# Kernel optimization log

Measured on AMD Instinct MI355X. Metric: run time of the kernel, lower is better.

The kernel has to match this reference:

```python
import jax, jax.numpy as jnp
import numpy as np

L, D, HID, QH, KVH, V, B, S, R = 2, 1024, 4096, 16, 4, 32000, 2, 2048, 20
HEAD, G = D // QH, QH // KVH
ALPHA, THETA = 32.0, 50000.0


def setup_inputs() -> dict:
    key = jax.random.key(0)
    ks = iter(jax.random.split(key, 40))
    def w(shape, s=0.02):
        return jax.random.normal(next(ks), shape, jnp.float32) * s
    KD = KVH * HEAD
    return {
        'xs': jax.random.randint(next(ks), (B, S), 0, V, dtype=jnp.int32),
        'emb': w((V, D)),
        'Wq': w((L, D, D)), 'bq': w((L, D)),
        'Wk': w((L, D, KD)), 'bk': w((L, KD)),
        'Wv': w((L, D, KD)), 'bv': w((L, KD)),
        'Wo': w((L, D, D)), 'bo': w((L, D)),
        'att_scale': 1.0 + w((L, D)),
        'mlp_scale': 1.0 + w((L, D)),
        'final_scale': 1.0 + w((D,)),
        'W1': w((L, D, HID)), 'A1': w((L, D, R)), 'a1b': w((L, R)), 'B1': w((L, R, HID)), 'b1b': w((L, HID)),
        'W2': w((L, D, HID)), 'A2': w((L, D, R)), 'a2b': w((L, R)), 'B2': w((L, R, HID)), 'b2b': w((L, HID)),
        'W3': w((L, HID, D)), 'A3': w((L, HID, R)), 'a3b': w((L, R)), 'B3': w((L, R, D)), 'b3b': w((L, D)),
        'startpos': 0,
    }


def _rms(x, scale):
    return scale * x * jax.lax.rsqrt(jnp.mean(x * x, axis=-1, keepdims=True) + 1e-5)


def _lora(x, Wl, Aw, ab, Bw, bb):
    # base linear output is detached in the original (no grad through it)
    return jax.lax.stop_gradient(x @ Wl) + ((x @ Aw + ab) @ Bw + bb) / ALPHA


def _forward(xs, startpos, emb, Wq, bq, Wk, bk, Wv, bv, Wo, bo,
             att_scale, mlp_scale, final_scale,
             W1, A1, a1b, B1, b1b, W2, A2, a2b, B2, b2b, W3, A3, a3b, B3, b3b):
    x = emb[xs]  # (B,S,D)
    # RoPE tables (head dim = D//QH, pairs rotated as complex numbers)
    freqs = 1.0 / THETA ** (jnp.arange(0, HEAD, 2, dtype=jnp.float32) / HEAD)  # (HEAD//2,)
    pos = jnp.arange(startpos, startpos + S, dtype=jnp.float32)
    ang = pos[:, None] * freqs[None, :]  # (S, HEAD//2)
    cos, sin = jnp.cos(ang), jnp.sin(ang)

    def rope(t):  # t: (B,S,H,HEAD)
        tr = t.reshape(t.shape[:-1] + (HEAD // 2, 2))
        t0, t1 = tr[..., 0], tr[..., 1]
        c, s = cos[None, :, None, :], sin[None, :, None, :]
        return jnp.stack((t0 * c - t1 * s, t0 * s + t1 * c), axis=-1).reshape(t.shape)

    causal = jnp.arange(S)[None, :] <= jnp.arange(S)[:, None]  # (Sq, Skv)
    inv_sqrt_d = np.float32(1.0 / np.sqrt(HEAD))
    for l in range(L):
        h = _rms(x, att_scale[l])
        q = rope((h @ Wq[l] + bq[l]).reshape(B, S, QH, HEAD))
        k = rope((h @ Wk[l] + bk[l]).reshape(B, S, KVH, HEAD))
        v = (h @ Wv[l] + bv[l]).reshape(B, S, KVH, HEAD)
        # GQA: q heads grouped per kv head (q head i uses kv head i//G); no explicit KV repeat
        qg = q.reshape(B, S, KVH, G, HEAD)
        scores = jnp.einsum('bskgd,btkd->bkgst', qg, k) * inv_sqrt_d
        if startpos == 0:
            scores = jnp.where(causal[None, None, None], scores, -jnp.inf)
        attn = jax.nn.softmax(scores, axis=-1)
        o = jnp.einsum('bkgst,btkd->bskgd', attn, v).reshape(B, S, D)
        x = x + (o @ Wo[l] + bo[l])
        h2 = _rms(x, mlp_scale[l])
        m = _lora(h2, W1[l], A1[l], a1b[l], B1[l], b1b[l]) * jax.nn.silu(
            _lora(h2, W2[l], A2[l], a2b[l], B2[l], b2b[l]))
        x = x + _lora(m, W3[l], A3[l], a3b[l], B3[l], b3b[l])
    f = _rms(x, final_scale)
    return f @ emb.T  # tied logits (B,S,V)


def reference(xs, emb, Wq, bq, Wk, bk, Wv, bv, Wo, bo, att_scale, mlp_scale, final_scale,
              W1, A1, a1b, B1, b1b, W2, A2, a2b, B2, b2b, W3, A3, a3b, B3, b3b, startpos):
    return _forward(xs, startpos, emb, Wq, bq, Wk, bk, Wv, bv, Wo, bo,
                    att_scale, mlp_scale, final_scale,
                    W1, A1, a1b, B1, b1b, W2, A2, a2b, B2, b2b, W3, A3, a3b, B3, b3b)
```

## Files before the change

kernel.cpp:

```cpp
#include <hip/hip_runtime.h>
#include <hip/hip_bf16.h>
#include <math.h>

constexpr int L_   = 2;
constexpr int D_   = 1024;
constexpr int HID_ = 4096;
constexpr int QH_  = 16;
constexpr int KVH_ = 4;
constexpr int V_   = 32000;
constexpr int B_   = 2;
constexpr int S_   = 2048;
constexpr int R_   = 20;
constexpr int HEAD_ = D_ / QH_;
constexpr int KD_   = KVH_ * HEAD_;
constexpr int QKV_  = D_ + 2 * KD_;
constexpr int M_    = B_ * S_;
constexpr float INV_ALPHA_ = 1.0f / 32.0f;
constexpr float LOG_STEP_ = 0.3381180865f;

typedef unsigned short ushort_t;
typedef __attribute__((ext_vector_type(8))) short bf16x8;
typedef __attribute__((ext_vector_type(4))) float f32x4;
typedef __attribute__((address_space(1))) const unsigned int gas_u32;
typedef __attribute__((address_space(3))) unsigned int las_u32;

__device__ __forceinline__ void gload16(const void* g, void* l) {
  __builtin_amdgcn_global_load_lds((gas_u32*)g, (las_u32*)l, 16, 0, 0);
}

__device__ __forceinline__ ushort_t f2bf(float f) {
  union { float f; unsigned int u; } c; c.f = f;
  unsigned int u = c.u + 0x7FFFu + ((c.u >> 16) & 1u);
  return (ushort_t)(u >> 16);
}
__device__ __forceinline__ float bflo(unsigned int w) {
  union { unsigned int u; float f; } c; c.u = w << 16; return c.f;
}
__device__ __forceinline__ float bfhi(unsigned int w) {
  union { unsigned int u; float f; } c; c.u = w & 0xFFFF0000u; return c.f;
}

__global__ __launch_bounds__(256) void k_embed(const int* __restrict__ xs,
                                               const float* __restrict__ emb,
                                               float* __restrict__ x) {
  int i = blockIdx.x * blockDim.x + threadIdx.x;
  int total4 = M_ * D_ / 4;
  if (i >= total4) return;
  int row = i >> 8;
  int c4  = i & 255;
  const float4* src = reinterpret_cast<const float4*>(emb + (size_t)xs[row] * D_) + c4;
  reinterpret_cast<float4*>(x)[i] = *src;
}

__global__ __launch_bounds__(256) void k_rms(const float* __restrict__ x,
                                             const float* __restrict__ scale,
                                             ushort_t* __restrict__ out) {
  int row = blockIdx.x;
  const float* xr = x + (size_t)row * D_;
  float ss = 0.f;
  for (int i = threadIdx.x; i < D_; i += 256) { float v = xr[i]; ss += v * v; }
  for (int off = 32; off > 0; off >>= 1) ss += __shfl_down(ss, off);
  __shared__ float red[5];
  if ((threadIdx.x & 63) == 0) red[threadIdx.x >> 6] = ss;
  __syncthreads();
  if (threadIdx.x == 0)
    red[4] = rsqrtf((red[0] + red[1] + red[2] + red[3]) * (1.0f / D_) + 1e-5f);
  __syncthreads();
  float inv = red[4];
  ushort_t* orow = out + (size_t)row * D_;
  for (int i = threadIdx.x; i < D_; i += 256) orow[i] = f2bf(scale[i] * xr[i] * inv);
}

__global__ __launch_bounds__(256) void k_cast(const float* __restrict__ in,
                                              ushort_t* __restrict__ out, int n8) {
  int i = blockIdx.x * blockDim.x + threadIdx.x;
  if (i >= n8) return;
  const float4* p = reinterpret_cast<const float4*>(in) + i * 2;
  float4 a = p[0], b = p[1];
  ushort_t r[8] = { f2bf(a.x), f2bf(a.y), f2bf(a.z), f2bf(a.w),
                    f2bf(b.x), f2bf(b.y), f2bf(b.z), f2bf(b.w) };
  reinterpret_cast<uint4*>(out)[i] = *reinterpret_cast<uint4*>(r);
}

__global__ __launch_bounds__(256) void k_tcast(const float* __restrict__ in,
                                               ushort_t* __restrict__ out,
                                               int K, int N) {
  __shared__ float t[32][33];
  int n0 = blockIdx.x * 32, k0 = blockIdx.y * 32;
  int c = threadIdx.x & 31, r0 = threadIdx.x >> 5;
#pragma unroll
  for (int rr = 0; rr < 4; ++rr) {
    int r = r0 + rr * 8;
    t[r][c] = in[(size_t)(k0 + r) * N + n0 + c];
  }
  __syncthreads();
#pragma unroll
  for (int rr = 0; rr < 4; ++rr) {
    int r = r0 + rr * 8;
    out[(size_t)(n0 + r) * K + k0 + c] = f2bf(t[c][r]);
  }
}

__global__ __launch_bounds__(256) void k_qkvbias(const float* __restrict__ bq,
                                                 const float* __restrict__ bk,
                                                 const float* __restrict__ bv,
                                                 float* __restrict__ b) {
  int i = blockIdx.x * 256 + threadIdx.x;
  if (i >= QKV_) return;
  b[i] = i < D_ ? bq[i] : (i < D_ + KD_ ? bk[i - D_] : bv[i - D_ - KD_]);
}

__global__ __launch_bounds__(256) void k_ropeprep_k(const float* __restrict__ qkv,
                                                    ushort_t* __restrict__ Kb) {
  int i = blockIdx.x * 256 + threadIdx.x;
  int pi = i & 31;
  int kh = (i >> 5) & 3;
  int s  = (i >> 7) & (S_ - 1);
  int b  = i >> 18;
  float freq = expf(-LOG_STEP_ * (float)pi);
  float ang = (float)s * freq;
  float sn, cs;
  sincosf(ang, &sn, &cs);
  const float* p = qkv + (size_t)(b * S_ + s) * QKV_ + D_ + kh * 64 + 2 * pi;
  float t0 = p[0], t1 = p[1];
  ushort_t* q = Kb + (size_t)((b * KVH_ + kh) * S_ + s) * 64 + 2 * pi;
  q[0] = f2bf(t0 * cs - t1 * sn);
  q[1] = f2bf(t0 * sn + t1 * cs);
}

__global__ __launch_bounds__(256) void k_prep_v(const float* __restrict__ qkv,
                                                ushort_t* __restrict__ Vt) {
  __shared__ float t[32][33];
  int s0 = blockIdx.x * 32, d0 = blockIdx.y * 32, bkh = blockIdx.z;
  int c = threadIdx.x & 31, r0 = threadIdx.x >> 5;
#pragma unroll
  for (int rr = 0; rr < 4; ++rr) {
    int r = r0 + rr * 8;
    t[r][c] = qkv[(size_t)((bkh >> 2) * S_ + s0 + r) * QKV_ + D_ + KD_ + (bkh & 3) * 64 + d0 + c];
  }
  __syncthreads();
#pragma unroll
  for (int rr = 0; rr < 4; ++rr) {
    int r = r0 + rr * 8;
    Vt[(size_t)(bkh * 64 + d0 + r) * S_ + s0 + c] = f2bf(t[c][r]);
  }
}

__global__ __launch_bounds__(256) void k_attn3(const float* __restrict__ qkv,
                                               const ushort_t* __restrict__ Kb,
                                               const ushort_t* __restrict__ Vt,
                                               ushort_t* __restrict__ obf) {
  __shared__ ushort_t Ks[64 * 64];
  __shared__ ushort_t Vs[64 * 64];
  __shared__ ushort_t Ps[4][16 * 64];

  int bid = blockIdx.x;
  int qt = 31 - (bid & 31);
  int qh = (bid >> 5) & 15;
  int b  = bid >> 9;
  int kh = qh >> 2;
  int tid = threadIdx.x;
  int w = tid >> 6, lane = tid & 63;
  int q0 = qt * 64;

  const ushort_t* Kbh = Kb + (size_t)(b * KVH_ + kh) * S_ * 64;
  const ushort_t* Vth = Vt + (size_t)(b * KVH_ + kh) * 64 * S_;

  bf16x8 qa[2];
  {
    int pos = q0 + w * 16 + (lane & 15);
    const float* qp = qkv + (size_t)(b * S_ + pos) * QKV_ + qh * 64 + (lane >> 4) * 8;
#pragma unroll
    for (int kk = 0; kk < 2; ++kk) {
      float4 f0 = *reinterpret_cast<const float4*>(qp + kk * 32);
      float4 f1 = *reinterpret_cast<const float4*>(qp + kk * 32 + 4);
      float f[8] = {f0.x, f0.y, f0.z, f0.w, f1.x, f1.y, f1.z, f1.w};
      int dbase = (lane >> 4) * 8 + kk * 32;
      ushort_t tq[8];
#pragma unroll
      for (int p = 0; p < 4; ++p) {
        int pi = (dbase >> 1) + p;
        float freq = expf(-LOG_STEP_ * (float)pi);
        float ang = (float)pos * freq;
        float sn, cs;
        sincosf(ang, &sn, &cs);
        float t0 = f[2 * p], t1 = f[2 * p + 1];
        tq[2 * p]     = f2bf((t0 * cs - t1 * sn) * 0.125f);
        tq[2 * p + 1] = f2bf((t0 * sn + t1 * cs) * 0.125f);
      }
      qa[kk] = *reinterpret_cast<const bf16x8*>(tq);
    }
  }

  f32x4 oacc[4];
#pragma unroll
  for (int j = 0; j < 4; ++j) oacc[j] = {0.f, 0.f, 0.f, 0.f};
  float m[4] = {-1e30f, -1e30f, -1e30f, -1e30f};
  float l[4] = {0.f, 0.f, 0.f, 0.f};

  const int srow = lane >> 3;
  const int soff = ((lane & 7) ^ srow) * 16;

  for (int t0 = 0; t0 <= q0; t0 += 64) {
#pragma unroll
    for (int r = 0; r < 2; ++r) {
      int c = w * 2 + r;
      const char* gk = (const char*)Kbh + (size_t)(t0 + c * 8 + srow) * 128 + soff;
      gload16(gk, (char*)Ks + c * 1024);
      const char* gv = (const char*)Vth + (size_t)(c * 8 + srow) * (S_ * 2) + (size_t)t0 * 2 + soff;
      gload16(gv, (char*)Vs + c * 1024);
    }
    __syncthreads();

    f32x4 sacc[4];
#pragma unroll
    for (int j = 0; j < 4; ++j) sacc[j] = {0.f, 0.f, 0.f, 0.f};
#pragma unroll
    for (int kk = 0; kk < 2; ++kk) {
#pragma unroll
      for (int j = 0; j < 4; ++j) {
        int krow = j * 16 + (lane & 15);
        int chunk = kk * 4 + (lane >> 4);
        bf16x8 kf = *reinterpret_cast<const bf16x8*>(
            &Ks[krow * 64 + ((chunk ^ (krow & 7)) << 3)]);
        sacc[j] = __builtin_amdgcn_mfma_f32_16x16x32_bf16(qa[kk], kf, sacc[j], 0, 0, 0);
      }
    }
    if (t0 == q0) {
#pragma unroll
      for (int j = 0; j < 4; ++j)
#pragma unroll
        for (int e = 0; e < 4; ++e) {
          int keyr = j * 16 + (lane & 15);
          int qr = w * 16 + (lane >> 4) * 4 + e;
          if (keyr > qr) sacc[j][e] = -1e30f;
        }
    }

    float corr[4];
#pragma unroll
    for (int e = 0; e < 4; ++e) {
      float mt = fmaxf(fmaxf(sacc[0][e], sacc[1][e]), fmaxf(sacc[2][e], sacc[3][e]));
#pragma unroll
      for (int off = 1; off < 16; off <<= 1) mt = fmaxf(mt, __shfl_xor(mt, off));
      float mn = fmaxf(m[e], mt);
      corr[e] = __expf(m[e] - mn);
      m[e] = mn;
    }
    float rs[4] = {0.f, 0.f, 0.f, 0.f};
#pragma unroll
    for (int j = 0; j < 4; ++j)
#pragma unroll
      for (int e = 0; e < 4; ++e) {
        float p = __expf(sacc[j][e] - m[e]);
        sacc[j][e] = p;
        rs[e] += p;
      }
#pragma unroll
    for (int e = 0; e < 4; ++e) {
#pragma unroll
      for (int off = 1; off < 16; off <<= 1) rs[e] += __shfl_xor(rs[e], off);
      l[e] = l[e] * corr[e] + rs[e];
    }
#pragma unroll
    for (int j = 0; j < 4; ++j)
#pragma unroll
      for (int e = 0; e < 4; ++e) oacc[j][e] *= corr[e];

#pragma unroll
    for (int j = 0; j < 4; ++j)
#pragma unroll
      for (int e = 0; e < 4; ++e) {
        int prow = (lane >> 4) * 4 + e;
        int pcol = j * 16 + (lane & 15);
        Ps[w][prow * 64 + (((pcol >> 3) ^ (prow & 7)) << 3) + (pcol & 7)] = f2bf(sacc[j][e]);
      }

    bf16x8 pa[2];
    int prow2 = lane & 15;
#pragma unroll
    for (int kk = 0; kk < 2; ++kk) {
      int chunk = kk * 4 + (lane >> 4);
      pa[kk] = *reinterpret_cast<const bf16x8*>(
          &Ps[w][prow2 * 64 + ((chunk ^ (prow2 & 7)) << 3)]);
    }
#pragma unroll
    for (int kk = 0; kk < 2; ++kk) {
#pragma unroll
      for (int jd = 0; jd < 4; ++jd) {
        int vrow = jd * 16 + (lane & 15);
        int chunk = kk * 4 + (lane >> 4);
        bf16x8 vf = *reinterpret_cast<const bf16x8*>(
            &Vs[vrow * 64 + ((chunk ^ (vrow & 7)) << 3)]);
        oacc[jd] = __builtin_amdgcn_mfma_f32_16x16x32_bf16(pa[kk], vf, oacc[jd], 0, 0, 0);
      }
    }
    __syncthreads();
  }

#pragma unroll
  for (int e = 0; e < 4; ++e) {
    int tok = b * S_ + q0 + w * 16 + (lane >> 4) * 4 + e;
    float inv = 1.f / l[e];
#pragma unroll
    for (int jd = 0; jd < 4; ++jd) {
      int col = qh * 64 + jd * 16 + (lane & 15);
      obf[(size_t)tok * D_ + col] = f2bf(oacc[jd][e] * inv);
    }
  }
}

__global__ __launch_bounds__(256) void k_silumul(const ushort_t* __restrict__ g1,
                                                 const ushort_t* __restrict__ g2,
                                                 ushort_t* __restrict__ out) {
  int i = blockIdx.x * 256 + threadIdx.x;
  uint4 a4 = reinterpret_cast<const uint4*>(g1)[i];
  uint4 b4 = reinterpret_cast<const uint4*>(g2)[i];
  unsigned au[4] = {a4.x, a4.y, a4.z, a4.w};
  unsigned bu[4] = {b4.x, b4.y, b4.z, b4.w};
  ushort_t r[8];
#pragma unroll
  for (int q = 0; q < 4; ++q) {
    float a0 = bflo(au[q]), a1 = bfhi(au[q]);
    float b0 = bflo(bu[q]), b1 = bfhi(bu[q]);
    r[2 * q]     = f2bf(a0 * b0 / (1.f + __expf(-b0)));
    r[2 * q + 1] = f2bf(a1 * b1 / (1.f + __expf(-b1)));
  }
  reinterpret_cast<uint4*>(out)[i] = *reinterpret_cast<uint4*>(r);
}

__global__ __launch_bounds__(256) void k_trA(const float* __restrict__ A,
                                             ushort_t* __restrict__ At, int K) {
  int idx = blockIdx.x * 256 + threadIdx.x;
  if (idx >= K * R_) return;
  int k = idx / R_, r = idx - k * R_;
  At[(size_t)r * K + k] = f2bf(A[idx]);
}

template <int K>
__global__ __launch_bounds__(256) void k_loraA(const ushort_t* __restrict__ hbm,
                                               const ushort_t* __restrict__ At,
                                               const float* __restrict__ ab,
                                               float* __restrict__ u) {
  constexpr int E = K / 64;
  int row = blockIdx.x * 4 + (threadIdx.x >> 6);
  int lane = threadIdx.x & 63;
  float hf[E];
  {
    const uint4* hp = reinterpret_cast<const uint4*>(hbm + (size_t)row * K + lane * E);
#pragma unroll
    for (int i = 0; i < E / 8; ++i) {
      uint4 vv = hp[i];
      unsigned int wsv[4] = {vv.x, vv.y, vv.z, vv.w};
#pragma unroll
      for (int q = 0; q < 4; ++q) {
        hf[i * 8 + q * 2]     = bflo(wsv[q]);
        hf[i * 8 + q * 2 + 1] = bfhi(wsv[q]);
      }
    }
  }
  for (int r = 0; r < R_; ++r) {
    const uint4* ap = reinterpret_cast<const uint4*>(At + (size_t)r * K + lane * E);
    float acc = 0.f;
#pragma unroll
    for (int i = 0; i < E / 8; ++i) {
      uint4 av = ap[i];
      unsigned int wsv[4] = {av.x, av.y, av.z, av.w};
#pragma unroll
      for (int q = 0; q < 4; ++q) {
        acc = fmaf(hf[i * 8 + q * 2], bflo(wsv[q]), acc);
        acc = fmaf(hf[i * 8 + q * 2 + 1], bfhi(wsv[q]), acc);
      }
    }
#pragma unroll
    for (int off = 1; off < 64; off <<= 1) acc += __shfl_xor(acc, off);
    if (lane == 0) u[(size_t)row * R_ + r] = acc + ab[r];
  }
}

template <bool LORA, bool OBF, bool NTS>
__global__ __launch_bounds__(256) void k_bgemm(const ushort_t* __restrict__ A,
                                               const ushort_t* __restrict__ Bt,
                                               const float* __restrict__ bias,
                                               const float* __restrict__ u,
                                               const float* __restrict__ Bl,
                                               const float* __restrict__ lb,
                                               const float* __restrict__ Cin,
                                               void* __restrict__ Cout,
                                               int M, int N, int K) {
  __shared__ ushort_t lds[3][2][128 * 32];
  const int tid = threadIdx.x;
  const int lane = tid & 63;
  const int w = tid >> 6;
  const int wr = w >> 1, wc = w & 1;

  unsigned nwg = gridDim.x * gridDim.y;
  unsigned orig = blockIdx.y * gridDim.x + blockIdx.x;
  unsigned qq = nwg >> 3, r8 = nwg & 7;
  unsigned xcd = orig & 7, loc = orig >> 3;
  unsigned swz = (xcd < r8 ? xcd * (qq + 1) : r8 * (qq + 1) + (xcd - r8) * qq) + loc;
  const int bm = (int)(swz / gridDim.x) * 128;
  const int bn = (int)(swz % gridDim.x) * 128;

  f32x4 acc[4][4];
#pragma unroll
  for (int i = 0; i < 4; ++i)
#pragma unroll
    for (int j = 0; j < 4; ++j) acc[i][j] = {0.f, 0.f, 0.f, 0.f};

  const int srow = (lane >> 2);
  const int skcol = (lane & 3) * 8;
  const int nt = K >> 5;

#define STAGE_TILE(kt)                                                          \
  {                                                                             \
    int k0_ = (kt) * 32;                                                        \
    int sl_ = (kt) % 3;                                                         \
    _Pragma("unroll")                                                           \
    for (int q_ = 0; q_ < 2; ++q_) {                                            \
      int c_ = w * 2 + q_;                                                      \
      gload16(A + (size_t)(bm + c_ * 16 + srow) * K + k0_ + skcol,              \
              (char*)&lds[sl_][0][0] + c_ * 1024);                              \
      gload16(Bt + (size_t)(bn + c_ * 16 + srow) * K + k0_ + skcol,             \
              (char*)&lds[sl_][1][0] + c_ * 1024);                              \
    }                                                                           \
  }

  STAGE_TILE(0)
  STAGE_TILE(1)
  asm volatile("s_waitcnt vmcnt(4)\n\ts_barrier" ::: "memory");

  const int koff = (lane >> 4) * 8;
  const int rsel = lane & 15;

  for (int t = 0; t < nt; ++t) {
    if (t + 2 < nt) STAGE_TILE(t + 2)
    const ushort_t* As = &lds[t % 3][0][0];
    const ushort_t* Bs = &lds[t % 3][1][0];
    bf16x8 af[4], bfr[4];
#pragma unroll
    for (int i = 0; i < 4; ++i)
      af[i] = *reinterpret_cast<const bf16x8*>(&As[(wr * 64 + i * 16 + rsel) * 32 + koff]);
#pragma unroll
    for (int j = 0; j < 4; ++j)
      bfr[j] = *reinterpret_cast<const bf16x8*>(&Bs[(wc * 64 + j * 16 + rsel) * 32 + koff]);
    __builtin_amdgcn_s_setprio(1);
#pragma unroll
    for (int i = 0; i < 4; ++i)
#pragma unroll
      for (int j = 0; j < 4; ++j)
        acc[i][j] = __builtin_amdgcn_mfma_f32_16x16x32_bf16(af[i], bfr[j], acc[i][j], 0, 0, 0);
    __builtin_amdgcn_s_setprio(0);
    if (t + 2 < nt) {
      asm volatile("s_waitcnt vmcnt(4)\n\ts_barrier" ::: "memory");
    } else if (t + 1 < nt) {
      asm volatile("s_waitcnt vmcnt(0)\n\ts_barrier" ::: "memory");
    }
  }
#undef STAGE_TILE

  float* Cf = (float*)Cout;
  ushort_t* Cb = (ushort_t*)Cout;

  if constexpr (LORA) {
    asm volatile("s_barrier" ::: "memory");
    float* Us  = (float*)&lds[0][0][0];
    float* Bls = (float*)&lds[1][0][0];
    for (int t = tid; t < 128 * R_; t += 256) {
      Us[t] = u[(size_t)bm * R_ + t];
      int rr = t >> 7, nn = t & 127;
      Bls[t] = Bl[(size_t)rr * N + bn + nn];
    }
    __syncthreads();
#pragma unroll
    for (int i = 0; i < 4; ++i) {
      int rl0 = wr * 64 + i * 16 + (lane >> 4) * 4;
#pragma unroll
      for (int e = 0; e < 4; ++e) {
        int rl = rl0 + e;
        float u20[R_];
#pragma unroll
        for (int r = 0; r < R_; ++r) u20[r] = Us[rl * R_ + r];
#pragma unroll
        for (int j = 0; j < 4; ++j) {
          int cl = wc * 64 + j * 16 + (lane & 15);
          float ud = lb[bn + cl];
#pragma unroll
          for (int r = 0; r < R_; ++r) ud = fmaf(u20[r], Bls[r * 128 + cl], ud);
          int row = bm + rl, col = bn + cl;
          float vv = acc[i][j][e] + ud * INV_ALPHA_;
          if constexpr (OBF) {
            Cb[(size_t)row * N + col] = f2bf(vv);
          } else {
            if (Cin) vv += Cin[(size_t)row * N + col];
            Cf[(size_t)row * N + col] = vv;
          }
        }
      }
    }
  } else {
#pragma unroll
    for (int i = 0; i < 4; ++i) {
      int row0 = bm + wr * 64 + i * 16 + (lane >> 4) * 4;
#pragma unroll
      for (int j = 0; j < 4; ++j) {
        int col = bn + wc * 64 + j * 16 + (lane & 15);
        float bv = bias ? bias[col] : 0.f;
#pragma unroll
        for (int e = 0; e < 4; ++e) {
          int row = row0 + e;
          float vv = acc[i][j][e] + bv;
          if constexpr (OBF) {
            Cb[(size_t)row * N + col] = f2bf(vv);
          } else {
            if (Cin) vv += Cin[(size_t)row * N + col];
            if constexpr (NTS) {
              __builtin_nontemporal_store(vv, &Cf[(size_t)row * N + col]);
            } else {
              Cf[(size_t)row * N + col] = vv;
            }
          }
        }
      }
    }
  }
}

static inline void bgemm(hipStream_t st, const ushort_t* A, const ushort_t* Bt,
                         const float* bias, const float* Cin, float* C,
                         int M, int N, int K, bool nts = false) {
  dim3 g(N / 128, M / 128);
  if (nts)
    k_bgemm<false, false, true><<<g, 256, 0, st>>>(A, Bt, bias, nullptr, nullptr, nullptr, Cin, C, M, N, K);
  else
    k_bgemm<false, false, false><<<g, 256, 0, st>>>(A, Bt, bias, nullptr, nullptr, nullptr, Cin, C, M, N, K);
}
static inline void bgemm_lora_bf(hipStream_t st, const ushort_t* A, const ushort_t* Bt,
                                 const float* u, const float* Bl, const float* lb,
                                 ushort_t* C, int M, int N, int K) {
  dim3 g(N / 128, M / 128);
  k_bgemm<true, true, false><<<g, 256, 0, st>>>(A, Bt, nullptr, u, Bl, lb, nullptr, C, M, N, K);
}
static inline void bgemm_lora_f32(hipStream_t st, const ushort_t* A, const ushort_t* Bt,
                                  const float* u, const float* Bl, const float* lb,
                                  const float* Cin, float* C, int M, int N, int K) {
  dim3 g(N / 128, M / 128);
  k_bgemm<true, false, false><<<g, 256, 0, st>>>(A, Bt, nullptr, u, Bl, lb, Cin, C, M, N, K);
}
static inline void tcast(hipStream_t st, const float* in, ushort_t* out, int K, int N) {
  dim3 g(N / 32, K / 32);
  k_tcast<<<g, 256, 0, st>>>(in, out, K, N);
}

extern "C" void kernel_launch(void* const* d_in, const int* in_sizes, int n_in,
                              void* d_out, int out_size, void* d_ws, size_t ws_size,
                              hipStream_t stream) {
  (void)in_sizes; (void)n_in; (void)out_size; (void)ws_size;
  const int*   xs  = (const int*)d_in[0];
  const float* emb = (const float*)d_in[1];
  const float* Wq  = (const float*)d_in[2];
  const float* bq  = (const float*)d_in[3];
  const float* Wk  = (const float*)d_in[4];
  const float* bk  = (const float*)d_in[5];
  const float* Wv  = (const float*)d_in[6];
  const float* bv  = (const float*)d_in[7];
  const float* Wo  = (const float*)d_in[8];
  const float* bo  = (const float*)d_in[9];
  const float* att_scale   = (const float*)d_in[10];
  const float* mlp_scale   = (const float*)d_in[11];
  const float* final_scale = (const float*)d_in[12];
  const float* W1  = (const float*)d_in[13];
  const float* A1  = (const float*)d_in[14];
  const float* a1b = (const float*)d_in[15];
  const float* B1  = (const float*)d_in[16];
  const float* b1b = (const float*)d_in[17];
  const float* W2  = (const float*)d_in[18];
  const float* A2  = (const float*)d_in[19];
  const float* a2b = (const float*)d_in[20];
  const float* B2  = (const float*)d_in[21];
  const float* b2b = (const float*)d_in[22];
  const float* W3  = (const float*)d_in[23];
  const float* A3  = (const float*)d_in[24];
  const float* a3b = (const float*)d_in[25];
  const float* B3  = (const float*)d_in[26];
  const float* b3b = (const float*)d_in[27];
  float* out = (float*)d_out;

  float* ws   = (float*)d_ws;
  float* xbuf = ws;
  float* qkv  = xbuf + (size_t)M_ * D_;
  float* ubuf = qkv + (size_t)M_ * QKV_;
  float* qkvb = ubuf + (size_t)M_ * R_;
  ushort_t* g1b = (ushort_t*)(qkvb + QKV_);
  ushort_t* g2b = g1b + (size_t)M_ * HID_;
  ushort_t* hb  = g2b + (size_t)M_ * HID_;
  ushort_t* wT  = hb + (size_t)M_ * HID_;
  ushort_t* At  = wT + (size_t)HID_ * D_;
  ushort_t* embT = At + (size_t)R_ * HID_;
  ushort_t* Kb = g1b;
  ushort_t* Vt = Kb + (size_t)B_ * KVH_ * S_ * 64;

  k_embed<<<dim3(M_ * D_ / 4 / 256), dim3(256), 0, stream>>>(xs, emb, xbuf);

  for (int l = 0; l < L_; ++l) {
    k_rms<<<dim3(M_), dim3(256), 0, stream>>>(xbuf, att_scale + (size_t)l * D_, hb);
    tcast(stream, Wq + (size_t)l * D_ * D_, wT, D_, D_);
    tcast(stream, Wk + (size_t)l * D_ * KD_, wT + (size_t)D_ * D_, D_, KD_);
    tcast(stream, Wv + (size_t)l * D_ * KD_, wT + (size_t)(D_ + KD_) * D_, D_, KD_);
    k_qkvbias<<<dim3(6), dim3(256), 0, stream>>>(bq + (size_t)l * D_, bk + (size_t)l * KD_,
                                                 bv + (size_t)l * KD_, qkvb);
    bgemm(stream, hb, wT, qkvb, nullptr, qkv, M_, QKV_, D_);
    {
      int npk = M_ * KVH_ * 32;
      k_ropeprep_k<<<dim3(npk / 256), dim3(256), 0, stream>>>(qkv, Kb);
    }
    k_prep_v<<<dim3(S_ / 32, 2, B_ * KVH_), dim3(256), 0, stream>>>(qkv, Vt);
    k_attn3<<<dim3(B_ * QH_ * (S_ / 64)), dim3(256), 0, stream>>>(qkv, Kb, Vt, hb);
    tcast(stream, Wo + (size_t)l * D_ * D_, wT, D_, D_);
    bgemm(stream, hb, wT, bo + (size_t)l * D_, xbuf, xbuf, M_, D_, D_);

    k_rms<<<dim3(M_), dim3(256), 0, stream>>>(xbuf, mlp_scale + (size_t)l * D_, hb);
    k_trA<<<dim3((D_ * R_ + 255) / 256), dim3(256), 0, stream>>>(A1 + (size_t)l * D_ * R_, At, D_);
    k_loraA<D_><<<dim3(M_ / 4), dim3(256), 0, stream>>>(hb, At, a1b + (size_t)l * R_, ubuf);
    tcast(stream, W1 + (size_t)l * D_ * HID_, wT, D_, HID_);
    bgemm_lora_bf(stream, hb, wT, ubuf, B1 + (size_t)l * R_ * HID_, b1b + (size_t)l * HID_,
                  g1b, M_, HID_, D_);
    k_trA<<<dim3((D_ * R_ + 255) / 256), dim3(256), 0, stream>>>(A2 + (size_t)l * D_ * R_, At, D_);
    k_loraA<D_><<<dim3(M_ / 4), dim3(256), 0, stream>>>(hb, At, a2b + (size_t)l * R_, ubuf);
    tcast(stream, W2 + (size_t)l * D_ * HID_, wT, D_, HID_);
    bgemm_lora_bf(stream, hb, wT, ubuf, B2 + (size_t)l * R_ * HID_, b2b + (size_t)l * HID_,
                  g2b, M_, HID_, D_);
    k_silumul<<<dim3(M_ * HID_ / 8 / 256), dim3(256), 0, stream>>>(g1b, g2b, hb);
    k_trA<<<dim3((HID_ * R_ + 255) / 256), dim3(256), 0, stream>>>(A3 + (size_t)l * HID_ * R_, At, HID_);
    k_loraA<HID_><<<dim3(M_ / 4), dim3(256), 0, stream>>>(hb, At, a3b + (size_t)l * R_, ubuf);
    tcast(stream, W3 + (size_t)l * HID_ * D_, wT, HID_, D_);
    bgemm_lora_f32(stream, hb, wT, ubuf, B3 + (size_t)l * R_ * D_, b3b + (size_t)l * D_,
                   xbuf, xbuf, M_, D_, HID_);
  }

  k_rms<<<dim3(M_), dim3(256), 0, stream>>>(xbuf, final_scale, hb);
  {
    int n8 = (int)((size_t)V_ * D_ / 8);
    k_cast<<<dim3((n8 + 255) / 256), dim3(256), 0, stream>>>(emb, embT, n8);
  }
  bgemm(stream, hb, embT, nullptr, nullptr, out, M_, V_, D_, true);
}
```

Measured before the change: 1.802 ms.

## Add 256x128-tile, 512-thread GEMM with 64-wide K stages for MLP and logits

Adds a new GEMM kernel, k_bgemm2, that uses 256x128 output tiles, 8 waves, 64-deep K slices, XOR-swizzled LDS and triple-buffered async loads. It is used for the W1/W2 LoRA projections and the large vocabulary logits GEMM. The goal is more operand reuse per tile and fewer barriers per K step. It also drops the nontemporal store path for the logits output. Larger tiles raise LDS and register pressure and leave fewer workgroups for occupancy.

Result: faster. 1.566 ms (-13.1%).

```diff
diff --git a/kernel.cpp b/kernel.cpp
--- a/kernel.cpp
+++ b/kernel.cpp
@@ -378,7 +378,7 @@
   }
 }
 
-template <bool LORA, bool OBF, bool NTS>
+template <bool LORA, bool OBF>
 __global__ __launch_bounds__(256) void k_bgemm(const ushort_t* __restrict__ A,
                                                const ushort_t* __restrict__ Bt,
                                                const float* __restrict__ bias,
@@ -514,11 +514,7 @@
             Cb[(size_t)row * N + col] = f2bf(vv);
           } else {
             if (Cin) vv += Cin[(size_t)row * N + col];
-            if constexpr (NTS) {
-              __builtin_nontemporal_store(vv, &Cf[(size_t)row * N + col]);
-            } else {
-              Cf[(size_t)row * N + col] = vv;
-            }
+            Cf[(size_t)row * N + col] = vv;
           }
         }
       }
@@ -526,26 +522,186 @@
   }
 }
 
+template <bool LORA, bool OBF>
+__global__ __launch_bounds__(512, 2) void k_bgemm2(const ushort_t* __restrict__ A,
+                                                   const ushort_t* __restrict__ Bt,
+                                                   const float* __restrict__ bias,
+                                                   const float* __restrict__ u,
+                                                   const float* __restrict__ Bl,
+                                                   const float* __restrict__ lb,
+                                                   const float* __restrict__ Cin,
+                                                   void* __restrict__ Cout,
+                                                   int M, int N, int K) {
+  __shared__ ushort_t lds[3][24576];
+  const int tid = threadIdx.x;
+  const int lane = tid & 63;
+  const int w = tid >> 6;
+  const int wr = w >> 1;
+  const int wc = w & 1;
+
+  unsigned nwg = gridDim.x * gridDim.y;
+  unsigned orig = blockIdx.y * gridDim.x + blockIdx.x;
+  unsigned qq = nwg >> 3, r8 = nwg & 7;
+  unsigned xcd = orig & 7, loc = orig >> 3;
+  unsigned swz = (xcd < r8 ? xcd * (qq + 1) : r8 * (qq + 1) + (xcd - r8) * qq) + loc;
+  const int bm = (int)(swz / gridDim.x) * 256;
+  const int bn = (int)(swz % gridDim.x) * 128;
+
+  f32x4 acc[4][4];
+#pragma unroll
+  for (int i = 0; i < 4; ++i)
+#pragma unroll
+    for (int j = 0; j < 4; ++j) acc[i][j] = {0.f, 0.f, 0.f, 0.f};
+
+  const int srow8 = lane >> 3;
+  const int scol  = ((lane & 7) ^ srow8) * 8;
+  const int nt = K >> 6;
+
+#define STAGE2(kt)                                                              \
+  {                                                                             \
+    int k0_ = (kt) << 6;                                                        \
+    int sl_ = (kt) % 3;                                                         \
+    _Pragma("unroll")                                                           \
+    for (int c_ = 0; c_ < 4; ++c_) {                                            \
+      int ch = w * 4 + c_;                                                      \
+      gload16(A + (size_t)(bm + ch * 8 + srow8) * K + k0_ + scol,               \
+              (char*)&lds[sl_][0] + ch * 1024);                                 \
+    }                                                                           \
+    _Pragma("unroll")                                                           \
+    for (int c_ = 0; c_ < 2; ++c_) {                                            \
+      int ch = w * 2 + c_;                                                      \
+      gload16(Bt + (size_t)(bn + ch * 8 + srow8) * K + k0_ + scol,              \
+              (char*)&lds[sl_][16384] + ch * 1024);                             \
+    }                                                                           \
+  }
+
+  STAGE2(0)
+  STAGE2(1)
+  asm volatile("s_waitcnt vmcnt(6)\n\ts_barrier" ::: "memory");
+
+  const int rsel = lane & 15;
+  const int g4 = lane >> 4;
+
+  for (int t = 0; t < nt; ++t) {
+    if (t + 2 < nt) STAGE2(t + 2)
+    const ushort_t* As = &lds[t % 3][0];
+    const ushort_t* Bs = &lds[t % 3][16384];
+#pragma unroll
+    for (int kk = 0; kk < 2; ++kk) {
+      int slotA = kk * 4 + g4;
+      bf16x8 af[4], bfr[4];
+#pragma unroll
+      for (int fm = 0; fm < 4; ++fm) {
+        int row = wr * 64 + fm * 16 + rsel;
+        af[fm] = *reinterpret_cast<const bf16x8*>(&As[row * 64 + ((slotA ^ (row & 7)) << 3)]);
+      }
+#pragma unroll
+      for (int fn = 0; fn < 4; ++fn) {
+        int row = wc * 64 + fn * 16 + rsel;
+        bfr[fn] = *reinterpret_cast<const bf16x8*>(&Bs[row * 64 + ((slotA ^ (row & 7)) << 3)]);
+      }
+      __builtin_amdgcn_s_setprio(1);
+#pragma unroll
+      for (int fm = 0; fm < 4; ++fm)
+#pragma unroll
+        for (int fn = 0; fn < 4; ++fn)
+          acc[fm][fn] = __builtin_amdgcn_mfma_f32_16x16x32_bf16(af[fm], bfr[fn], acc[fm][fn], 0, 0, 0);
+      __builtin_amdgcn_s_setprio(0);
+    }
+    if (t + 2 < nt) {
+      asm volatile("s_waitcnt vmcnt(6)\n\ts_barrier" ::: "memory");
+    } else if (t + 1 < nt) {
+      asm volatile("s_waitcnt vmcnt(0)\n\ts_barrier" ::: "memory");
+    }
+  }
+#undef STAGE2
+
+  float* Cf = (float*)Cout;
+  ushort_t* Cb = (ushort_t*)Cout;
+
+  if constexpr (LORA) {
+    asm volatile("s_barrier" ::: "memory");
+    float* Us  = (float*)&lds[0][0];
+    float* Bls = (float*)&lds[1][0];
+    for (int t2 = tid; t2 < 256 * R_; t2 += 512) Us[t2] = u[(size_t)bm * R_ + t2];
+    for (int t2 = tid; t2 < R_ * 128; t2 += 512) {
+      int rr = t2 >> 7, nn = t2 & 127;
+      Bls[t2] = Bl[(size_t)rr * N + bn + nn];
+    }
+    __syncthreads();
+#pragma unroll
+    for (int fm = 0; fm < 4; ++fm) {
+      int rl0 = wr * 64 + fm * 16 + g4 * 4;
+#pragma unroll
+      for (int e = 0; e < 4; ++e) {
+        int rl = rl0 + e;
+        float u20[R_];
+#pragma unroll
+        for (int r = 0; r < R_; ++r) u20[r] = Us[rl * R_ + r];
+#pragma unroll
+        for (int fn = 0; fn < 4; ++fn) {
+          int cl = wc * 64 + fn * 16 + rsel;
+          float ud = lb[bn + cl];
+#pragma unroll
+          for (int r = 0; r < R_; ++r) ud = fmaf(u20[r], Bls[r * 128 + cl], ud);
+          int row = bm + rl, col = bn + cl;
+          float vv = acc[fm][fn][e] + ud * INV_ALPHA_;
+          if constexpr (OBF) {
+            Cb[(size_t)row * N + col] = f2bf(vv);
+          } else {
+            if (Cin) vv += Cin[(size_t)row * N + col];
+            Cf[(size_t)row * N + col] = vv;
+          }
+        }
+      }
+    }
+  } else {
+#pragma unroll
+    for (int fm = 0; fm < 4; ++fm) {
+      int row0 = bm + wr * 64 + fm * 16 + g4 * 4;
+#pragma unroll
+      for (int fn = 0; fn < 4; ++fn) {
+        int col = bn + wc * 64 + fn * 16 + rsel;
+        float bv = bias ? bias[col] : 0.f;
+#pragma unroll
+        for (int e = 0; e < 4; ++e) {
+          int row = row0 + e;
+          float vv = acc[fm][fn][e] + bv;
+          if constexpr (OBF) {
+            Cb[(size_t)row * N + col] = f2bf(vv);
+          } else {
+            if (Cin) vv += Cin[(size_t)row * N + col];
+            Cf[(size_t)row * N + col] = vv;
+          }
+        }
+      }
+    }
+  }
+}
+
 static inline void bgemm(hipStream_t st, const ushort_t* A, const ushort_t* Bt,
                          const float* bias, const float* Cin, float* C,
-                         int M, int N, int K, bool nts = false) {
+                         int M, int N, int K) {
   dim3 g(N / 128, M / 128);
-  if (nts)
-    k_bgemm<false, false, true><<<g, 256, 0, st>>>(A, Bt, bias, nullptr, nullptr, nullptr, Cin, C, M, N, K);
-  else
-    k_bgemm<false, false, false><<<g, 256, 0, st>>>(A, Bt, bias, nullptr, nullptr, nullptr, Cin, C, M, N, K);
-}
-static inline void bgemm_lora_bf(hipStream_t st, const ushort_t* A, const ushort_t* Bt,
-                                 const float* u, const float* Bl, const float* lb,
-                                 ushort_t* C, int M, int N, int K) {
-  dim3 g(N / 128, M / 128);
-  k_bgemm<true, true, false><<<g, 256, 0, st>>>(A, Bt, nullptr, u, Bl, lb, nullptr, C, M, N, K);
+  k_bgemm<false, false><<<g, 256, 0, st>>>(A, Bt, bias, nullptr, nullptr, nullptr, Cin, C, M, N, K);
 }
 static inline void bgemm_lora_f32(hipStream_t st, const ushort_t* A, const ushort_t* Bt,
                                   const float* u, const float* Bl, const float* lb,
                                   const float* Cin, float* C, int M, int N, int K) {
   dim3 g(N / 128, M / 128);
-  k_bgemm<true, false, false><<<g, 256, 0, st>>>(A, Bt, nullptr, u, Bl, lb, Cin, C, M, N, K);
+  k_bgemm<true, false><<<g, 256, 0, st>>>(A, Bt, nullptr, u, Bl, lb, Cin, C, M, N, K);
+}
+static inline void bgemm2(hipStream_t st, const ushort_t* A, const ushort_t* Bt,
+                          const float* bias, const float* Cin, float* C,
+                          int M, int N, int K) {
+  dim3 g(N / 128, M / 256);
+  k_bgemm2<false, false><<<g, 512, 0, st>>>(A, Bt, bias, nullptr, nullptr, nullptr, Cin, C, M, N, K);
+}
+static inline void bgemm2_lora_bf(hipStream_t st, const ushort_t* A, const ushort_t* Bt,
+                                  const float* u, const float* Bl, const float* lb,
+                                  ushort_t* C, int M, int N, int K) {
+  dim3 g(N / 128, M / 256);
+  k_bgemm2<true, true><<<g, 512, 0, st>>>(A, Bt, nullptr, u, Bl, lb, nullptr, C, M, N, K);
 }
 static inline void tcast(hipStream_t st, const float* in, ushort_t* out, int K, int N) {
   dim3 g(N / 32, K / 32);
@@ -623,13 +779,13 @@
     k_trA<<<dim3((D_ * R_ + 255) / 256), dim3(256), 0, stream>>>(A1 + (size_t)l * D_ * R_, At, D_);
     k_loraA<D_><<<dim3(M_ / 4), dim3(256), 0, stream>>>(hb, At, a1b + (size_t)l * R_, ubuf);
     tcast(stream, W1 + (size_t)l * D_ * HID_, wT, D_, HID_);
-    bgemm_lora_bf(stream, hb, wT, ubuf, B1 + (size_t)l * R_ * HID_, b1b + (size_t)l * HID_,
-                  g1b, M_, HID_, D_);
+    bgemm2_lora_bf(stream, hb, wT, ubuf, B1 + (size_t)l * R_ * HID_, b1b + (size_t)l * HID_,
+                   g1b, M_, HID_, D_);
     k_trA<<<dim3((D_ * R_ + 255) / 256), dim3(256), 0, stream>>>(A2 + (size_t)l * D_ * R_, At, D_);
     k_loraA<D_><<<dim3(M_ / 4), dim3(256), 0, stream>>>(hb, At, a2b + (size_t)l * R_, ubuf);
     tcast(stream, W2 + (size_t)l * D_ * HID_, wT, D_, HID_);
-    bgemm_lora_bf(stream, hb, wT, ubuf, B2 + (size_t)l * R_ * HID_, b2b + (size_t)l * HID_,
-                  g2b, M_, HID_, D_);
+    bgemm2_lora_bf(stream, hb, wT, ubuf, B2 + (size_t)l * R_ * HID_, b2b + (size_t)l * HID_,
+                   g2b, M_, HID_, D_);
     k_silumul<<<dim3(M_ * HID_ / 8 / 256), dim3(256), 0, stream>>>(g1b, g2b, hb);
     k_trA<<<dim3((HID_ * R_ + 255) / 256), dim3(256), 0, stream>>>(A3 + (size_t)l * HID_ * R_, At, HID_);
     k_loraA<HID_><<<dim3(M_ / 4), dim3(256), 0, stream>>>(hb, At, a3b + (size_t)l * R_, ubuf);
@@ -643,5 +799,5 @@
     int n8 = (int)((size_t)V_ * D_ / 8);
     k_cast<<<dim3((n8 + 255) / 256), dim3(256), 0, stream>>>(emb, embT, n8);
   }
-  bgemm(stream, hb, embT, nullptr, nullptr, out, M_, V_, D_, true);
-}
+  bgemm2(stream, hb, embT, nullptr, nullptr, out, M_, V_, D_);
+}
```
